# Performance work log

Hardware: AMD Instinct MI355X
Metric: run time of the kernel (lower is better)

The kernel has to match this reference:

```python
import jax, jax.numpy as jnp
import numpy as np

N_TOK = 256
C_Z = 128
C = 32
N_HEAD = 4


def setup_inputs() -> dict:
    key = jax.random.key(0)
    ks = jax.random.split(key, 8)
    s = 0.02
    return {
        "z": jax.random.normal(ks[0], (N_TOK, N_TOK, C_Z), dtype=jnp.float32),
        "single_mask": jnp.ones((N_TOK,), dtype=jnp.float32),
        "ln_gamma": jnp.ones((C_Z,), dtype=jnp.float32),
        "ln_beta": jnp.zeros((C_Z,), dtype=jnp.float32),
        "W_q": jax.random.normal(ks[1], (C_Z, N_HEAD * C), dtype=jnp.float32) * s,
        "W_k": jax.random.normal(ks[2], (C_Z, N_HEAD * C), dtype=jnp.float32) * s,
        "W_v": jax.random.normal(ks[3], (C_Z, N_HEAD * C), dtype=jnp.float32) * s,
        "W_b": jax.random.normal(ks[4], (C_Z, N_HEAD), dtype=jnp.float32) * s,
        "W_g": jax.random.normal(ks[5], (C_Z, N_HEAD * C), dtype=jnp.float32) * s,
        "W_out": jax.random.normal(ks[6], (N_HEAD * C, C_Z), dtype=jnp.float32) * s,
    }


def reference(z, single_mask, ln_gamma, ln_beta, W_q, W_k, W_v, W_b, W_g, W_out):
    # LayerNorm over c_z
    mu = jnp.mean(z, axis=-1, keepdims=True)
    var = jnp.var(z, axis=-1, keepdims=True)
    zn = (z - mu) * jax.lax.rsqrt(var + 1e-5) * ln_gamma + ln_beta

    n = zn.shape[0]
    proj = lambda W: (zn @ W).reshape(n, n, N_HEAD, C)
    q = proj(W_q)
    k = proj(W_k)
    v = proj(W_v)
    g = proj(W_g)
    b = zn @ W_b  # [i, j, h] -> used as bias b[j, k, h]

    # a[i,j,k,h] = q[i,j]·k[i,k]/sqrt(c) + b[j,k,h]
    a = jnp.einsum('ijhc,ikhc->ijkh', q, k) / np.sqrt(C).astype(np.float32)
    a = a + b[None, :, :, :]
    a = a + (-1e9) * (1.0 - single_mask)[None, None, :, None]
    a = jax.nn.softmax(a, axis=-2)  # over k

    o = jnp.einsum('ijkh,ikhc->ijhc', a, v)
    o = jax.nn.sigmoid(g) * o
    o = o.reshape(n, n, N_HEAD * C)
    return o @ W_out
```

## Files before the change

kernel.cpp:

```cpp
#include <hip/hip_runtime.h>
#include <hip/hip_bf16.h>

#define NT 256
#define CZ 128
#define CH 32
#define NH 4
#define PL 2097152

typedef unsigned short ushort_t;
typedef unsigned int uint_t;
typedef __attribute__((ext_vector_type(8))) short short8;
typedef __attribute__((ext_vector_type(4))) float f32x4;

__device__ __forceinline__ float bfbits2f(uint_t bits){
  union { uint_t u; float f; } v; v.u = bits; return v.f;
}
__device__ __forceinline__ float bf2f(ushort_t u){
  return bfbits2f(((uint_t)u) << 16);
}
__device__ __forceinline__ ushort_t f2bf(float f){
  union { float f; uint_t u; } v; v.f = f;
  uint_t u = v.u;
  uint_t r = (u + 0x7fffu + ((u >> 16) & 1u)) >> 16;
  return (ushort_t)r;
}
__device__ __forceinline__ void unpk(uint_t w, float& lo, float& hi){
  lo = bfbits2f(w << 16);
  hi = bfbits2f(w & 0xffff0000u);
}
__device__ __forceinline__ short8 as_s8(uint4 u){
  union { uint4 u; short8 s; } v; v.u = u; return v.s;
}
__device__ __forceinline__ uint_t pk2(float a, float b){
  union { __hip_bfloat16 h; ushort_t u; } x, y;
  x.h = __float2bfloat16(a); y.h = __float2bfloat16(b);
  return (uint_t)x.u | ((uint_t)y.u << 16);
}
__device__ __forceinline__ int detect_f32(const ushort_t* zz){
  int l = threadIdx.x & 63;
  int bad = 0;
  #pragma unroll
  for(int s=0;s<4;s++){
    float v = bf2f(zz[l*4 + s]);
    if(!(fabsf(v) < 1e9f)) bad = 1;
  }
  return (__ballot(bad) != 0ull) ? 1 : 0;
}

__global__ void k_cvt_small(const void* __restrict__ m_, const void* __restrict__ g_,
    const void* __restrict__ b_, const void* __restrict__ wb_,
    float* __restrict__ dst, const ushort_t* __restrict__ zz){
  int isf32 = detect_f32(zz);
  int idx = threadIdx.x * 4;
  const void* sp; int off;
  if(idx < 256){ sp = m_;  off = idx; }
  else if(idx < 384){ sp = g_;  off = idx-256; }
  else if(idx < 512){ sp = b_;  off = idx-384; }
  else { sp = wb_; off = idx-512; }
  float4 o;
  if(isf32){ o = *(const float4*)((const float*)sp + off); }
  else {
    uint2 u = *(const uint2*)((const ushort_t*)sp + off);
    unpk(u.x, o.x, o.y); unpk(u.y, o.z, o.w);
  }
  *(float4*)(dst + idx) = o;
}

__global__ __launch_bounds__(256) void k_cvt_wt(const void* __restrict__ s0,
    const void* __restrict__ s1, const void* __restrict__ s2,
    const void* __restrict__ s3, const void* __restrict__ s4,
    ushort_t* __restrict__ dst, const ushort_t* __restrict__ zz){
  int isf32 = detect_f32(zz);
  const void* srcs[5] = {s0,s1,s2,s3,s4};
  int w = blockIdx.x >> 6;
  int idx = (blockIdx.x & 63)*256 + threadIdx.x;
  int k = idx >> 7, c = idx & 127;
  const void* sp = srcs[w];
  float v;
  if(isf32) v = ((const float*)sp)[idx];
  else      v = bf2f(((const ushort_t*)sp)[idx]);
  dst[(size_t)w*16384 + (size_t)c*128 + k] = f2bf(v);
}

__global__ __launch_bounds__(256) void k_lnproj(const void* __restrict__ zraw,
    const float* __restrict__ smallf, const ushort_t* __restrict__ Wt,
    ushort_t* __restrict__ qh, ushort_t* __restrict__ kh,
    ushort_t* __restrict__ vh, ushort_t* __restrict__ gh,
    float* __restrict__ btm){
  __shared__ __align__(16) char lds[47104];
  ushort_t* znl = (ushort_t*)lds;
  float*    tbB = (float*)(lds + 34816);
  float*    wbs = (float*)(lds + 45056);
  const float* mkf = smallf;
  const float* gmf = smallf + 256;
  const float* btf = smallf + 384;
  const float* Wbf = smallf + 512;
  int t = threadIdx.x;
  int isf32 = detect_f32((const ushort_t*)zraw);
  wbs[t] = Wbf[t]; wbs[t+256] = Wbf[t+256];
  __syncthreads();

  int row_loc = t >> 1, half = t & 1;
  size_t r = (size_t)blockIdx.x*128 + row_loc;
  float mval = -1e9f * (1.f - mkf[r & 255]);
  float s = 0.f, s2 = 0.f;
  if(isf32){
    const float4* zp = (const float4*)((const float*)zraw + r*CZ + half*64);
    #pragma unroll
    for(int q=0;q<16;q++){
      float4 v = zp[q];
      s  += (v.x + v.y) + (v.z + v.w);
      s2 += (v.x*v.x + v.y*v.y) + (v.z*v.z + v.w*v.w);
    }
  } else {
    const uint4* zp = (const uint4*)((const ushort_t*)zraw + r*CZ + half*64);
    #pragma unroll
    for(int q=0;q<8;q++){
      uint4 u = zp[q];
      const uint_t* pu = (const uint_t*)&u;
      #pragma unroll
      for(int e=0;e<4;e++){
        float lo, hi; unpk(pu[e], lo, hi);
        s += lo + hi; s2 += lo*lo + hi*hi;
      }
    }
  }
  s  += __shfl_xor(s, 1);
  s2 += __shfl_xor(s2, 1);
  float mu  = s * (1.f/CZ);
  float var = fmaxf(s2 * (1.f/CZ) - mu*mu, 0.f);
  float rs  = rsqrtf(var + 1e-5f);
  float acch[4] = {0.f,0.f,0.f,0.f};
  #pragma unroll
  for(int chunk=0;chunk<8;chunk++){
    float v8[8];
    if(isf32){
      const float4* zp = (const float4*)((const float*)zraw + r*CZ + half*64 + chunk*8);
      float4 a = zp[0], b = zp[1];
      v8[0]=a.x; v8[1]=a.y; v8[2]=a.z; v8[3]=a.w;
      v8[4]=b.x; v8[5]=b.y; v8[6]=b.z; v8[7]=b.w;
    } else {
      uint4 u = *(const uint4*)((const ushort_t*)zraw + r*CZ + half*64 + chunk*8);
      const uint_t* pu = (const uint_t*)&u;
      #pragma unroll
      for(int e=0;e<4;e++) unpk(pu[e], v8[e*2], v8[e*2+1]);
    }
    uint_t ow[4];
    #pragma unroll
    for(int e2=0;e2<4;e2++){
      int cg = half*64 + chunk*8 + e2*2;
      float v0 = (v8[e2*2]   - mu)*rs*gmf[cg]   + btf[cg];
      float v1 = (v8[e2*2+1] - mu)*rs*gmf[cg+1] + btf[cg+1];
      float4 w0 = *(const float4*)&wbs[cg*4];
      float4 w1 = *(const float4*)&wbs[(cg+1)*4];
      acch[0] += v0*w0.x + v1*w1.x;
      acch[1] += v0*w0.y + v1*w1.y;
      acch[2] += v0*w0.z + v1*w1.z;
      acch[3] += v0*w0.w + v1*w1.w;
      ow[e2] = (uint_t)f2bf(v0) | ((uint_t)f2bf(v1) << 16);
    }
    uint4 o; o.x=ow[0]; o.y=ow[1]; o.z=ow[2]; o.w=ow[3];
    *(uint4*)(znl + row_loc*136 + half*64 + chunk*8) = o;
  }
  #pragma unroll
  for(int h=0;h<4;h++){
    float tot = acch[h] + __shfl_xor(acch[h], 1);
    if(half == 0) btm[(size_t)h*65536 + r] = (tot + mval) * 1.4426950408889634f;
  }
  __syncthreads();

  int wave = t>>6, l = t&63, n = l&15, quad = l>>4;
  uint4 af[2][4];
  #pragma unroll
  for(int mt=0;mt<2;mt++)
    #pragma unroll
    for(int kb=0;kb<4;kb++)
      af[mt][kb] = *(const uint4*)(znl + (wave*32 + mt*16 + n)*136 + kb*32 + quad*8);
  float* T = tbB + wave*640;
  int rrow = l >> 1, rhalf = l & 1;
  ushort_t* outs[4] = {qh, kh, vh, gh};
  size_t row0 = (size_t)blockIdx.x*128 + wave*32;
  #pragma unroll
  for(int w=0;w<4;w++){
    const ushort_t* W = Wt + (size_t)w*16384;
    ushort_t* D = outs[w];
    float sc = (w==0) ? (0.17677669529663687f * 1.4426950408889634f) : 1.f;
    #pragma unroll
    for(int nt=0;nt<8;nt++){
      uint4 bfr[4];
      #pragma unroll
      for(int kb=0;kb<4;kb++)
        bfr[kb] = *(const uint4*)(W + ((size_t)(nt*16 + n))*128 + kb*32 + quad*8);
      f32x4 a0 = {0.f,0.f,0.f,0.f}, a1 = {0.f,0.f,0.f,0.f};
      #pragma unroll
      for(int kb=0;kb<4;kb++){
        a0 = __builtin_amdgcn_mfma_f32_16x16x32_bf16(as_s8(af[0][kb]), as_s8(bfr[kb]), a0, 0,0,0);
        a1 = __builtin_amdgcn_mfma_f32_16x16x32_bf16(as_s8(af[1][kb]), as_s8(bfr[kb]), a1, 0,0,0);
      }
      #pragma unroll
      for(int rr=0;rr<4;rr++){
        T[(quad*4 + rr)*20 + n]      = a0[rr];
        T[(16 + quad*4 + rr)*20 + n] = a1[rr];
      }
      float4 v0 = *(const float4*)(T + rrow*20 + rhalf*8);
      float4 v1 = *(const float4*)(T + rrow*20 + rhalf*8 + 4);
      uint4 o;
      o.x = (uint_t)f2bf(v0.x*sc) | ((uint_t)f2bf(v0.y*sc) << 16);
      o.y = (uint_t)f2bf(v0.z*sc) | ((uint_t)f2bf(v0.w*sc) << 16);
      o.z = (uint_t)f2bf(v1.x*sc) | ((uint_t)f2bf(v1.y*sc) << 16);
      o.w = (uint_t)f2bf(v1.z*sc) | ((uint_t)f2bf(v1.w*sc) << 16);
      *(uint4*)(D + (size_t)(nt>>1)*PL + (row0 + rrow)*CH + (nt&1)*16 + rhalf*8) = o;
    }
  }
}

__global__ __launch_bounds__(256) void k_attn(
    const ushort_t* __restrict__ qh, const ushort_t* __restrict__ kh,
    const ushort_t* __restrict__ vh, const ushort_t* __restrict__ gh,
    const float* __restrict__ btm, ushort_t* __restrict__ oh){
  __shared__ __align__(16) char lds[40960];
  uint4*    VfA = (uint4*)lds;
  uint4*    Kf  = (uint4*)(lds + 16384);
  ushort_t* Pw0 = (ushort_t*)(lds + 32768);
  int t = threadIdx.x;
  int i = blockIdx.x >> 2, h = blockIdx.x & 3;
  int wave = t >> 6, l = t & 63;
  int n = l & 15, quad = l >> 4;
  const ushort_t* qhp = qh + (size_t)h*PL + (size_t)(i*NT)*CH;
  const ushort_t* khp = kh + (size_t)h*PL + (size_t)(i*NT)*CH;
  const ushort_t* vhp = vh + (size_t)h*PL + (size_t)(i*NT)*CH;
  const ushort_t* ghp = gh + (size_t)h*PL + (size_t)(i*NT)*CH;
  ushort_t*       ohp = oh + (size_t)h*PL + (size_t)(i*NT)*CH;
  const float*    bth = btm + (size_t)h*65536;

  {
    #pragma unroll
    for(int m=0;m<4;m++){
      int kt = wave*4 + m;
      Kf[kt*64 + l] = *(const uint4*)(khp + (size_t)(kt*16 + n)*CH + quad*8);
    }
  }
  {
    #pragma unroll
    for(int it=0; it<4; it++){
      int u = wave + it*4, kblk = u >> 1, ct = u & 1;
      uint_t d[4];
      #pragma unroll
      for(int e=0;e<4;e++){
        uint_t lo = vhp[(size_t)(kblk*32 + quad*8 + e*2    )*CH + ct*16 + n];
        uint_t hi = vhp[(size_t)(kblk*32 + quad*8 + e*2 + 1)*CH + ct*16 + n];
        d[e] = lo | (hi << 16);
      }
      uint4 o; o.x=d[0]; o.y=d[1]; o.z=d[2]; o.w=d[3];
      VfA[u*64 + l] = o;
    }
  }
  __syncthreads();

  ushort_t* Pw = Pw0 + wave*1024;
  int swz = (n & 7) << 4;

  uint4 qf[4];
  uint2 gp0[4], gp1[4];
  #pragma unroll
  for(int s=0;s<4;s++){
    int jt = wave*4 + s;
    size_t rb = (size_t)(jt*16 + n)*CH;
    qf[s]  = *(const uint4*)(qhp + rb + quad*8);
    gp0[s] = *(const uint2*)(ghp + rb + quad*4);
    gp1[s] = *(const uint2*)(ghp + rb + 16 + quad*4);
  }

  #pragma unroll
  for(int s=0;s<4;s++){
    int jt = wave*4 + s;
    const float* brow = bth + (size_t)(jt*16 + n)*256 + quad*4;
    f32x4 oa0 = {0.f,0.f,0.f,0.f}, oa1 = {0.f,0.f,0.f,0.f};
    float sum0 = 0.f, sum1 = 0.f;
    #pragma unroll
    for(int Q=0;Q<4;Q++){
      f32x4 acc[4];
      #pragma unroll
      for(int m=0;m<4;m++)
        acc[m] = *(const f32x4*)(brow + (Q*4+m)*16);
      #pragma unroll
      for(int m=0;m<4;m++){
        uint4 kfv = Kf[(Q*4+m)*64 + l];
        acc[m] = __builtin_amdgcn_mfma_f32_16x16x32_bf16(as_s8(kfv), as_s8(qf[s]), acc[m], 0,0,0);
      }
      #pragma unroll
      for(int m=0;m<4;m++){
        float e0 = __builtin_amdgcn_exp2f(acc[m][0]);
        float e1 = __builtin_amdgcn_exp2f(acc[m][1]);
        float e2 = __builtin_amdgcn_exp2f(acc[m][2]);
        float e3 = __builtin_amdgcn_exp2f(acc[m][3]);
        sum0 += e0 + e1; sum1 += e2 + e3;
        uint2 pv;
        pv.x = pk2(e0, e1);
        pv.y = pk2(e2, e3);
        *(uint2*)((char*)Pw + (((n<<7) + (m<<5) + (quad<<3)) ^ swz)) = pv;
      }
      #pragma unroll
      for(int kb=0;kb<2;kb++){
        uint4 pf = *(const uint4*)((char*)Pw + (((n<<7) + (kb<<6) + (quad<<4)) ^ swz));
        int kg = Q*2 + kb;
        oa0 = __builtin_amdgcn_mfma_f32_16x16x32_bf16(as_s8(VfA[(kg*2+0)*64 + l]), as_s8(pf), oa0, 0,0,0);
        oa1 = __builtin_amdgcn_mfma_f32_16x16x32_bf16(as_s8(VfA[(kg*2+1)*64 + l]), as_s8(pf), oa1, 0,0,0);
      }
    }
    float ssum = sum0 + sum1;
    ssum += __shfl_xor(ssum, 16);
    ssum += __shfl_xor(ssum, 32);
    float inv = 1.f / ssum;
    size_t rb = (size_t)(jt*16 + n)*CH;
    float ga[4], gc[4];
    unpk(gp0[s].x, ga[0], ga[1]); unpk(gp0[s].y, ga[2], ga[3]);
    unpk(gp1[s].x, gc[0], gc[1]); unpk(gp1[s].y, gc[2], gc[3]);
    float v0[4], v1[4];
    #pragma unroll
    for(int rr=0;rr<4;rr++){
      v0[rr] = oa0[rr] * inv * (1.f/(1.f + __expf(-ga[rr])));
      v1[rr] = oa1[rr] * inv * (1.f/(1.f + __expf(-gc[rr])));
    }
    uint2 s0, s1;
    s0.x = (uint_t)f2bf(v0[0]) | ((uint_t)f2bf(v0[1]) << 16);
    s0.y = (uint_t)f2bf(v0[2]) | ((uint_t)f2bf(v0[3]) << 16);
    s1.x = (uint_t)f2bf(v1[0]) | ((uint_t)f2bf(v1[1]) << 16);
    s1.y = (uint_t)f2bf(v1[2]) | ((uint_t)f2bf(v1[3]) << 16);
    *(uint2*)(ohp + rb + quad*4)      = s0;
    *(uint2*)(ohp + rb + 16 + quad*4) = s1;
  }
}

__global__ __launch_bounds__(256) void k_gemm1(const ushort_t* __restrict__ oh,
    const ushort_t* __restrict__ Wt, void* __restrict__ outp,
    const ushort_t* __restrict__ zz){
  __shared__ __align__(16) float tbB[4*640];
  int isf32 = detect_f32(zz);
  int t = threadIdx.x, wave = t>>6, l = t&63, n = l&15, quad = l>>4;
  size_t row0 = (size_t)blockIdx.x*128 + wave*32;
  float* T = tbB + wave*640;
  int rrow = l >> 1, rhalf = l & 1;
  uint4 af[2][4];
  #pragma unroll
  for(int mt=0;mt<2;mt++)
    #pragma unroll
    for(int kb=0;kb<4;kb++)
      af[mt][kb] = *(const uint4*)(oh + (size_t)kb*PL + (row0 + mt*16 + n)*CH + quad*8);
  #pragma unroll
  for(int nt=0;nt<8;nt++){
    uint4 bfr[4];
    #pragma unroll
    for(int kb=0;kb<4;kb++)
      bfr[kb] = *(const uint4*)(Wt + ((size_t)(nt*16 + n))*128 + kb*32 + quad*8);
    f32x4 a0 = {0.f,0.f,0.f,0.f}, a1 = {0.f,0.f,0.f,0.f};
    #pragma unroll
    for(int kb=0;kb<4;kb++){
      a0 = __builtin_amdgcn_mfma_f32_16x16x32_bf16(as_s8(af[0][kb]), as_s8(bfr[kb]), a0, 0,0,0);
      a1 = __builtin_amdgcn_mfma_f32_16x16x32_bf16(as_s8(af[1][kb]), as_s8(bfr[kb]), a1, 0,0,0);
    }
    #pragma unroll
    for(int rr=0;rr<4;rr++){
      T[(quad*4 + rr)*20 + n]      = a0[rr];
      T[(16 + quad*4 + rr)*20 + n] = a1[rr];
    }
    float4 v0 = *(const float4*)(T + rrow*20 + rhalf*8);
    float4 v1 = *(const float4*)(T + rrow*20 + rhalf*8 + 4);
    if(isf32){
      float* of = (float*)outp + (row0 + rrow)*CZ + nt*16 + rhalf*8;
      *(float4*)of = v0;
      *(float4*)(of + 4) = v1;
    } else {
      uint4 o;
      o.x = (uint_t)f2bf(v0.x) | ((uint_t)f2bf(v0.y) << 16);
      o.y = (uint_t)f2bf(v0.z) | ((uint_t)f2bf(v0.w) << 16);
      o.z = (uint_t)f2bf(v1.x) | ((uint_t)f2bf(v1.y) << 16);
      o.w = (uint_t)f2bf(v1.z) | ((uint_t)f2bf(v1.w) << 16);
      *(uint4*)((ushort_t*)outp + (row0 + rrow)*CZ + nt*16 + rhalf*8) = o;
    }
  }
}

extern "C" void kernel_launch(void* const* d_in, const int* in_sizes, int n_in,
                              void* d_out, int out_size, void* d_ws, size_t ws_size,
                              hipStream_t stream){
  char* wsb = (char*)d_ws;
  const size_t TB = (size_t)16777216;
  ushort_t* qh  = (ushort_t*)(wsb);
  ushort_t* kh  = (ushort_t*)(wsb + TB);
  ushort_t* vh  = (ushort_t*)(wsb + 2*TB);
  ushort_t* gh  = (ushort_t*)(wsb + 3*TB);
  ushort_t* oh  = (ushort_t*)(wsb + 4*TB);
  float*    btm = (float*)   (wsb + 5*TB);
  float*  smallf= (float*)   (wsb + 5*TB + (1u<<20));
  ushort_t* Wt  = (ushort_t*)(wsb + 5*TB + (1u<<20) + 4096);
  const ushort_t* zz = (const ushort_t*)d_in[0];

  k_cvt_small<<<1,   256, 0, stream>>>(d_in[1], d_in[2], d_in[3], d_in[7], smallf, zz);
  k_cvt_wt   <<<320, 256, 0, stream>>>(d_in[4], d_in[5], d_in[6], d_in[8], d_in[9], Wt, zz);
  k_lnproj   <<<512, 256, 0, stream>>>(d_in[0], smallf, Wt, qh, kh, vh, gh, btm);
  k_attn     <<<1024,256, 0, stream>>>(qh, kh, vh, gh, btm, oh);
  k_gemm1    <<<512, 256, 0, stream>>>(oh, Wt + (size_t)4*16384, d_out, zz);
}
```

Baseline: 230.5 us.

## Batch all bias loads and QK MFMAs per row tile before exp and PV

Restructures the per-tile attention loop so that all 16 bias tiles are loaded up front, all 16 QK MFMAs are issued back-to-back, and all exponentials are computed before the PV stage. The outer loop is no longer unrolled, and the q and gate loads move inside it instead of being preloaded for all four tiles. The aim is to expose more memory-level and MFMA parallelism per tile while keeping register pressure bounded. The cost is 64 accumulator floats plus 32 packed values live at once, which could raise VGPR use and lower occupancy.

After: 220.0 us. 4.6% less time.

```diff
diff --git a/kernel.cpp b/kernel.cpp
--- a/kernel.cpp
+++ b/kernel.cpp
@@ -260,46 +260,37 @@
   ushort_t* Pw = Pw0 + wave*1024;
   int swz = (n & 7) << 4;
 
-  uint4 qf[4];
-  uint2 gp0[4], gp1[4];
-  #pragma unroll
+  #pragma unroll 1
   for(int s=0;s<4;s++){
     int jt = wave*4 + s;
-    size_t rb = (size_t)(jt*16 + n)*CH;
-    qf[s]  = *(const uint4*)(qhp + rb + quad*8);
-    gp0[s] = *(const uint2*)(ghp + rb + quad*4);
-    gp1[s] = *(const uint2*)(ghp + rb + 16 + quad*4);
-  }
-
-  #pragma unroll
-  for(int s=0;s<4;s++){
-    int jt = wave*4 + s;
-    const float* brow = bth + (size_t)(jt*16 + n)*256 + quad*4;
+    uint4 qf = *(const uint4*)(qhp + (size_t)(jt*16 + n)*CH + quad*8);
+    f32x4 acc[16];
+    #pragma unroll
+    for(int kt=0;kt<16;kt++)
+      acc[kt] = *(const f32x4*)(bth + (size_t)(jt*16 + n)*256 + kt*16 + quad*4);
+    #pragma unroll
+    for(int kt=0;kt<16;kt++){
+      uint4 kfv = Kf[kt*64 + l];
+      acc[kt] = __builtin_amdgcn_mfma_f32_16x16x32_bf16(as_s8(kfv), as_s8(qf), acc[kt], 0,0,0);
+    }
+    float sum0 = 0.f, sum1 = 0.f;
+    uint2 pv[16];
+    #pragma unroll
+    for(int kt=0;kt<16;kt++){
+      float e0 = __builtin_amdgcn_exp2f(acc[kt][0]);
+      float e1 = __builtin_amdgcn_exp2f(acc[kt][1]);
+      float e2 = __builtin_amdgcn_exp2f(acc[kt][2]);
+      float e3 = __builtin_amdgcn_exp2f(acc[kt][3]);
+      sum0 += e0 + e1; sum1 += e2 + e3;
+      pv[kt].x = pk2(e0, e1);
+      pv[kt].y = pk2(e2, e3);
+    }
     f32x4 oa0 = {0.f,0.f,0.f,0.f}, oa1 = {0.f,0.f,0.f,0.f};
-    float sum0 = 0.f, sum1 = 0.f;
     #pragma unroll
     for(int Q=0;Q<4;Q++){
-      f32x4 acc[4];
       #pragma unroll
       for(int m=0;m<4;m++)
-        acc[m] = *(const f32x4*)(brow + (Q*4+m)*16);
-      #pragma unroll
-      for(int m=0;m<4;m++){
-        uint4 kfv = Kf[(Q*4+m)*64 + l];
-        acc[m] = __builtin_amdgcn_mfma_f32_16x16x32_bf16(as_s8(kfv), as_s8(qf[s]), acc[m], 0,0,0);
-      }
-      #pragma unroll
-      for(int m=0;m<4;m++){
-        float e0 = __builtin_amdgcn_exp2f(acc[m][0]);
-        float e1 = __builtin_amdgcn_exp2f(acc[m][1]);
-        float e2 = __builtin_amdgcn_exp2f(acc[m][2]);
-        float e3 = __builtin_amdgcn_exp2f(acc[m][3]);
-        sum0 += e0 + e1; sum1 += e2 + e3;
-        uint2 pv;
-        pv.x = pk2(e0, e1);
-        pv.y = pk2(e2, e3);
-        *(uint2*)((char*)Pw + (((n<<7) + (m<<5) + (quad<<3)) ^ swz)) = pv;
-      }
+        *(uint2*)((char*)Pw + (((n<<7) + (m<<5) + (quad<<3)) ^ swz)) = pv[Q*4+m];
       #pragma unroll
       for(int kb=0;kb<2;kb++){
         uint4 pf = *(const uint4*)((char*)Pw + (((n<<7) + (kb<<6) + (quad<<4)) ^ swz));
@@ -313,9 +304,11 @@
     ssum += __shfl_xor(ssum, 32);
     float inv = 1.f / ssum;
     size_t rb = (size_t)(jt*16 + n)*CH;
+    uint2 g0 = *(const uint2*)(ghp + rb + quad*4);
+    uint2 g1 = *(const uint2*)(ghp + rb + 16 + quad*4);
     float ga[4], gc[4];
-    unpk(gp0[s].x, ga[0], ga[1]); unpk(gp0[s].y, ga[2], ga[3]);
-    unpk(gp1[s].x, gc[0], gc[1]); unpk(gp1[s].y, gc[2], gc[3]);
+    unpk(g0.x, ga[0], ga[1]); unpk(g0.y, ga[2], ga[3]);
+    unpk(g1.x, gc[0], gc[1]); unpk(g1.y, gc[2], gc[3]);
     float v0[4], v1[4];
     #pragma unroll
     for(int rr=0;rr<4;rr++){
```
